# Kernel optimization log

Measured on AMD Instinct MI355X. Metric: run time of the kernel, lower is better.

The kernel has to match this reference:

```python
import jax, jax.numpy as jnp
import numpy as np


def setup_inputs() -> dict:
    key = jax.random.key(0)
    k1, k2 = jax.random.split(key)
    x = jax.random.normal(k1, (3000, 800, 8), dtype=jnp.float32)
    y = jax.random.normal(k2, (3000, 800, 8), dtype=jnp.float32)
    return {"x": x, "y": y}


def _cumtrapz(a):
    # torch.cumulative_trapezoid along last axis (unit spacing): len nt-1
    return jnp.cumsum(0.5 * (a[:, 1:] + a[:, :-1]), axis=1)


def _wd1d(x, y):
    nt = x.shape[0]
    # flatten (ntraces, nchannels) -> batch of independent 1D traces [N, nt]
    syn = x.reshape(nt, -1).T
    obs = y.reshape(nt, -1).T
    # per trace-pair joint minimum (torch.min(torch.min(syn), torch.min(obs)))
    mind = jnp.minimum(syn.min(axis=1, keepdims=True), obs.min(axis=1, keepdims=True))
    syn = syn - mind
    obs = obs - mind
    cdf_syn = _cumtrapz(syn)                                  # [N, nt-1]
    cdf_obs = _cumtrapz(obs)                                  # [N, nt-1]
    syn_norm = cdf_syn / jnp.sum(cdf_syn, axis=1, keepdims=True)
    obs_norm = cdf_obs / jnp.sum(cdf_obs, axis=1, keepdims=True)
    # torch.searchsorted default (right=False) == jnp side='left'
    idx = jax.vmap(lambda a, v: jnp.searchsorted(a, v, side='left'))(obs_norm, syn_norm)
    idx = jnp.minimum(idx, nt - 1)                            # clamp; t[idx] == idx since t = arange(nt)
    t_tail = jnp.arange(1, nt, dtype=jnp.int32)               # t[1:]
    diff = (t_tail[None, :] - idx).astype(syn_norm.dtype)
    return jnp.sum(diff * diff * syn_norm)


def reference(x, y):
    return _wd1d(x, y)
```

## Files before the change

kernel.cpp:

```cpp
#include <hip/hip_runtime.h>

#define NT   3000
#define NK   2999
#define NTR  6400
#define TRIW 4498500.0f
#define FINF 3.4e38f

#define TSTR 3008
#define CB   47

__device__ __forceinline__ float wave_incl_scan(float v, int lane) {
    #pragma unroll
    for (int d = 1; d < 64; d <<= 1) {
        float t = __shfl_up(v, d);
        if (lane >= d) v += t;
    }
    return v;
}
__device__ __forceinline__ float wave_red_add(float v) {
    #pragma unroll
    for (int d = 1; d < 64; d <<= 1) v += __shfl_xor(v, d);
    return v;
}
__device__ __forceinline__ float wave_red_min(float v) {
    #pragma unroll
    for (int d = 1; d < 64; d <<= 1) v = fminf(v, __shfl_xor(v, d));
    return v;
}

__global__ __launch_bounds__(256) void kT(
    const float* __restrict__ X, const float* __restrict__ Y,
    float* __restrict__ sTx, float* __restrict__ sTy,
    float* __restrict__ mnx, float* __restrict__ mny,
    float* __restrict__ wsx, float* __restrict__ wsy)
{
    __shared__ float t[65][65];
    const int lane = threadIdx.x & 63;
    const int wv   = threadIdx.x >> 6;
    const int n0 = blockIdx.x * 64;
    const int j0 = blockIdx.y * 64;
    const int z  = blockIdx.z;
    const float* __restrict__ src = z ? Y : X;
    float* __restrict__ dst = z ? sTy : sTx;
    float* __restrict__ mnA = z ? mny : mnx;
    float* __restrict__ wsA = z ? wsy : wsx;

    #pragma unroll
    for (int i = 0; i < 17; ++i) {
        const int r = wv + 4 * i;
        if (r < 65) {
            const int jr = j0 + r;
            if (jr < NT) t[r][lane] = src[(size_t)jr * NTR + n0 + lane];
        }
    }
    __syncthreads();

    const int j = j0 + lane;
    const bool vs = (j < NK);
    const bool va = (j < NT);
    const float w = vs ? (float)(NK - j) : 0.f;

    for (int rr = 0; rr < 16; ++rr) {
        const int row = wv * 16 + rr;
        const float a0 = t[lane][row];
        const float a1 = t[lane + 1][row];
        const float s  = vs ? 0.5f * (a0 + a1) : 0.f;
        dst[(size_t)(n0 + row) * TSTR + j0 + lane] = s;
        const float ws = wave_red_add(s * w);
        const float mv = wave_red_min(va ? a0 : FINF);
        if (lane == 0) {
            wsA[blockIdx.y * NTR + n0 + row] = ws;
            mnA[blockIdx.y * NTR + n0 + row] = mv;
        }
    }
}

__global__ __launch_bounds__(256) void kB2(
    const float* __restrict__ mnx, const float* __restrict__ mny,
    const float* __restrict__ wsx, const float* __restrict__ wsy,
    float* __restrict__ mindA, float* __restrict__ SsA, float* __restrict__ SoA)
{
    const int n = blockIdx.x * 256 + threadIdx.x;
    float mn = FINF, sx = 0.f, sy = 0.f;
    for (int c = 0; c < CB; ++c) {
        const int o = c * NTR + n;
        mn = fminf(mn, fminf(mnx[o], mny[o]));
        sx += wsx[o]; sy += wsy[o];
    }
    mindA[n] = mn;
    SsA[n] = sx - mn * TRIW;
    SoA[n] = sy - mn * TRIW;
}

__global__ __launch_bounds__(256) void kC2(
    const float* __restrict__ sTx, const float* __restrict__ sTy,
    const float* __restrict__ mindA, const float* __restrict__ SsA,
    const float* __restrict__ SoA, float* __restrict__ partial)
{
    const int lane = threadIdx.x & 63;
    const int wv   = threadIdx.x >> 6;
    const int n = blockIdx.x * 4 + wv;

    const float mind = mindA[n];
    const float Ss = SsA[n];
    const float So = SoA[n];
    const float* __restrict__ sx_row = sTx + (size_t)n * TSTR;
    const float* __restrict__ sy_row = sTy + (size_t)n * TSTR;

    int   m0 = 0;
    float co = 0.f;
    float ov;

    #define REFILL() do {                                                   \
        const int mm = m0 + lane;                                           \
        float v_ = (mm < NK) ? sy_row[mm] : 0.f;                            \
        float pf_ = wave_incl_scan(v_, lane);                               \
        ov = (mm < NK) ? (co + pf_ - (float)(mm + 1) * mind) * Ss : FINF;   \
        co += __shfl(pf_, 63);                                              \
    } while (0)

    REFILL();

    float cs = 0.f, acc = 0.f;
    for (int b = 0; b < CB; ++b) {
        const int j = b * 64 + lane;
        const bool valid = (j < NK);
        float v = valid ? sx_row[j] : 0.f;
        float pf = wave_incl_scan(v, lane);
        const float synp = cs + pf - (float)(j + 1) * mind;
        cs += __shfl(pf, 63);
        const float target = valid ? synp * So : -FINF;

        bool pend = true;
        int idx = 0;
        while (true) {
            const float ov_top = __shfl(ov, 63);
            int lo = 0;
            #pragma unroll
            for (int s = 32; s; s >>= 1) {
                const float pv = __shfl(ov, lo + s - 1);
                if (pv < target) lo += s;
            }
            if (pend && (target <= ov_top)) { idx = m0 + lo; pend = false; }
            if (__all(!pend)) break;
            m0 += 64;
            REFILL();
        }
        if (valid) {
            const float diff = (float)(j + 1 - idx);
            acc = fmaf(diff * diff, synp, acc);
        }
    }
    #undef REFILL

    const float tot = wave_red_add(acc);
    __shared__ float red[4];
    if (lane == 0) red[wv] = tot / Ss;
    __syncthreads();
    if (threadIdx.x == 0)
        partial[blockIdx.x] = red[0] + red[1] + red[2] + red[3];
}

__global__ __launch_bounds__(256) void kD(
    const float* __restrict__ partial, float* __restrict__ out)
{
    float v = 0.f;
    for (int i = threadIdx.x; i < 1600; i += 256) v += partial[i];
    __shared__ float red[256];
    red[threadIdx.x] = v;
    __syncthreads();
    for (int s = 128; s > 0; s >>= 1) {
        if (threadIdx.x < s) red[threadIdx.x] += red[threadIdx.x + s];
        __syncthreads();
    }
    if (threadIdx.x == 0) out[0] = red[0];
}

#define NPAIR  3200
#define FCH    64
#define FKCH   47
#define GRP    8
#define GT     64

__global__ __launch_bounds__(128) void fA(
    const float* __restrict__ X, const float* __restrict__ Y,
    float* __restrict__ offx, float* __restrict__ offy,
    float* __restrict__ cmn,
    float* __restrict__ wsxA, float* __restrict__ wsyA)
{
    const int p = blockIdx.x * 128 + threadIdx.x;
    const int n = 2 * p;
    const int c = blockIdx.y;
    const int j0 = c * FKCH;
    const int j1 = min(NK, j0 + FKCH);

    const float2* __restrict__ X2 = (const float2*)X;
    const float2* __restrict__ Y2 = (const float2*)Y;

    float2 xp = X2[j0 * NPAIR + p];
    float2 yp = Y2[j0 * NPAIR + p];
    float mn0 = fminf(xp.x, yp.x), mn1 = fminf(xp.y, yp.y);
    float sx0 = 0.f, sx1 = 0.f, sy0 = 0.f, sy1 = 0.f;
    float wx0 = 0.f, wx1 = 0.f, wy0 = 0.f, wy1 = 0.f;

    #pragma unroll 8
    for (int j = j0; j < j1; ++j) {
        const float2 xn = X2[(j + 1) * NPAIR + p];
        const float2 yn = Y2[(j + 1) * NPAIR + p];
        const float w = (float)(NK - j);
        float s;
        s = 0.5f * (xp.x + xn.x); sx0 += s; wx0 = fmaf(s, w, wx0);
        s = 0.5f * (xp.y + xn.y); sx1 += s; wx1 = fmaf(s, w, wx1);
        s = 0.5f * (yp.x + yn.x); sy0 += s; wy0 = fmaf(s, w, wy0);
        s = 0.5f * (yp.y + yn.y); sy1 += s; wy1 = fmaf(s, w, wy1);
        mn0 = fminf(mn0, fminf(xn.x, yn.x));
        mn1 = fminf(mn1, fminf(xn.y, yn.y));
        xp = xn; yp = yn;
    }

    const int o = c * NTR + n;
    *(float2*)&offx[o] = make_float2(sx0, sx1);
    *(float2*)&offy[o] = make_float2(sy0, sy1);
    *(float2*)&cmn[o]  = make_float2(mn0, mn1);
    atomicAdd(&wsxA[n], wx0); atomicAdd(&wsxA[n + 1], wx1);
    atomicAdd(&wsyA[n], wy0); atomicAdd(&wsyA[n + 1], wy1);
}

__global__ __launch_bounds__(256) void fB(
    float* __restrict__ offx, float* __restrict__ offy,
    const float* __restrict__ cmn,
    const float* __restrict__ wsxA, const float* __restrict__ wsyA,
    float* __restrict__ mindA, float* __restrict__ SsynA,
    float* __restrict__ SobsA, float* __restrict__ out)
{
    __shared__ float tA[FCH][GT + 1];
    __shared__ float tB[FCH][GT + 1];

    const int n0 = blockIdx.x * GT;
    const int tid = threadIdx.x;
    const int lane = tid & 63;
    const int crow = tid >> 6;
    if (blockIdx.x == 0 && tid == 0) out[0] = 0.0f;

    for (int c = crow; c < FCH; c += 4)
        tB[c][lane] = cmn[c * NTR + n0 + lane];
    __syncthreads();
    if (tid < GT) {
        float mn = FINF;
        for (int c = 0; c < FCH; ++c) mn = fminf(mn, tB[c][tid]);
        mindA[n0 + tid] = mn;
        SsynA[n0 + tid] = wsxA[n0 + tid] - mn * TRIW;
        SobsA[n0 + tid] = wsyA[n0 + tid] - mn * TRIW;
    }
    __syncthreads();

    for (int c = crow; c < FCH; c += 4) {
        tA[c][lane] = offx[c * NTR + n0 + lane];
        tB[c][lane] = offy[c * NTR + n0 + lane];
    }
    __syncthreads();
    if (tid < GT) {
        float rx = 0.f, ry = 0.f;
        for (int c = 0; c < FCH; ++c) {
            const float tx = tA[c][tid], ty = tB[c][tid];
            tA[c][tid] = rx; tB[c][tid] = ry;
            rx += tx; ry += ty;
        }
    }
    __syncthreads();
    for (int c = crow; c < FCH; c += 4) {
        offx[c * NTR + n0 + lane] = tA[c][lane];
        offy[c * NTR + n0 + lane] = tB[c][lane];
    }
}

__global__ __launch_bounds__(256) void fC(
    const float* __restrict__ X, const float* __restrict__ Y,
    const float* __restrict__ offx, const float* __restrict__ offy,
    const float* __restrict__ mindA, const float* __restrict__ SsynA,
    const float* __restrict__ SobsA, float* __restrict__ out)
{
    const int n = blockIdx.x * 256 + threadIdx.x;
    const int c = blockIdx.y;
    const int j0 = c * FKCH;
    const int j1 = min(NK, j0 + FKCH);

    const float mind = mindA[n];
    const float Ssyn = SsynA[n];
    const float Sobs = SobsA[n];
    const float invS = 1.0f / Ssyn;

    float cs = offx[c * NTR + n];
    float xp = X[j0 * NTR + n];
    float acc = 0.f;

    int   mbase;
    float co, ylast;
    float o[GRP];
    float co8, y8;

    #define FILL() do {                                                   \
        float yl_ = ylast, cc_ = co;                                      \
        _Pragma("unroll")                                                 \
        for (int i = 0; i < GRP; ++i) {                                   \
            const int m_ = mbase + i;                                     \
            const int ml_ = (m_ < NK) ? (m_ + 1) : NK;                    \
            const float yn_ = Y[ml_ * NTR + n];                           \
            cc_ += 0.5f * (yl_ + yn_);                                    \
            yl_ = yn_;                                                    \
            const float v_ = (cc_ - (float)(m_ + 1) * mind) * Ssyn;       \
            o[i] = (m_ < NK) ? v_ : FINF;                                 \
        }                                                                 \
        co8 = cc_; y8 = yl_;                                              \
    } while (0)

    #define COUNT(tgt, cnt) do {                                          \
        cnt = 0;                                                          \
        _Pragma("unroll")                                                 \
        for (int i = 0; i < GRP; ++i) cnt += (o[i] < (tgt)) ? 1 : 0;      \
    } while (0)

    {
        const float xn = X[(j0 + 1) * NTR + n];
        cs += 0.5f * (xp + xn); xp = xn;
        const float synp = cs - (float)(j0 + 1) * mind;
        const float target = synp * Sobs;

        int cc = 0;
        for (int c2 = min(FCH - 1, c + 2); c2 >= 1; --c2) {
            const float v = (offy[c2 * NTR + n] - (float)(c2 * FKCH) * mind) * Ssyn;
            if (v < target) { cc = c2; break; }
        }
        mbase = cc * FKCH;
        co = offy[cc * NTR + n];
        ylast = Y[mbase * NTR + n];
        FILL();
        int cnt; COUNT(target, cnt);
        while (cnt == GRP) {
            mbase += GRP; co = co8; ylast = y8;
            FILL();
            COUNT(target, cnt);
        }
        const float diff = (float)(j0 + 1 - (mbase + cnt));
        acc = fmaf(diff * diff, synp, acc);
    }

    for (int k = j0 + 1; k < j1; ++k) {
        const float xn = X[(k + 1) * NTR + n];
        cs += 0.5f * (xp + xn); xp = xn;
        const float synp = cs - (float)(k + 1) * mind;
        const float target = synp * Sobs;

        int cnt; COUNT(target, cnt);
        while (cnt == GRP) {
            mbase += GRP; co = co8; ylast = y8;
            FILL();
            COUNT(target, cnt);
        }
        const float diff = (float)(k + 1 - (mbase + cnt));
        acc = fmaf(diff * diff, synp, acc);
    }
    acc *= invS;

    #undef FILL
    #undef COUNT

    __shared__ float red[256];
    red[threadIdx.x] = acc;
    __syncthreads();
    for (int s = 128; s > 0; s >>= 1) {
        if (threadIdx.x < s) red[threadIdx.x] += red[threadIdx.x + s];
        __syncthreads();
    }
    if (threadIdx.x == 0) atomicAdd(out, red[0]);
}

extern "C" void kernel_launch(void* const* d_in, const int* in_sizes, int n_in,
                              void* d_out, int out_size, void* d_ws, size_t ws_size,
                              hipStream_t stream)
{
    const float* X = (const float*)d_in[0];
    const float* Y = (const float*)d_in[1];
    float* out = (float*)d_out;

    const size_t NEW_REQ =
        ((size_t)2 * NTR * TSTR + 4 * (size_t)CB * NTR + 3 * NTR + 1600) * 4;

    if (ws_size >= NEW_REQ) {
        float* w = (float*)d_ws;
        float* sTx = w;
        float* sTy = sTx + (size_t)NTR * TSTR;
        float* mnx = sTy + (size_t)NTR * TSTR;
        float* mny = mnx + CB * NTR;
        float* wsx = mny + CB * NTR;
        float* wsy = wsx + CB * NTR;
        float* mindA = wsy + CB * NTR;
        float* SsA = mindA + NTR;
        float* SoA = SsA + NTR;
        float* partial = SoA + NTR;

        kT<<<dim3(100, 47, 2), 256, 0, stream>>>(X, Y, sTx, sTy, mnx, mny, wsx, wsy);
        kB2<<<25, 256, 0, stream>>>(mnx, mny, wsx, wsy, mindA, SsA, SoA);
        kC2<<<1600, 256, 0, stream>>>(sTx, sTy, mindA, SsA, SoA, partial);
        kD<<<1, 256, 0, stream>>>(partial, out);
    } else {
        float* w = (float*)d_ws;
        float* offx  = w;
        float* offy  = offx + FCH * NTR;
        float* cmn   = offy + FCH * NTR;
        float* wsxA  = cmn  + FCH * NTR;
        float* wsyA  = wsxA + NTR;
        float* mindA = wsyA + NTR;
        float* SsynA = mindA + NTR;
        float* SobsA = SsynA + NTR;

        hipMemsetAsync(wsxA, 0, 2 * NTR * sizeof(float), stream);

        dim3 gA(NPAIR / 128, FCH), bA(128);
        dim3 gB(NTR / GT), bB(256);
        dim3 gC(NTR / 256, FCH), bC(256);
        fA<<<gA, bA, 0, stream>>>(X, Y, offx, offy, cmn, wsxA, wsyA);
        fB<<<gB, bB, 0, stream>>>(offx, offy, cmn, wsxA, wsyA,
                                  mindA, SsynA, SobsA, out);
        fC<<<gC, bC, 0, stream>>>(X, Y, offx, offy, mindA, SsynA, SobsA, out);
    }
}
```

Measured before the change: 358.6 us.

## Split per-trace Wasserstein scan into segments with precomputed chunk prefixes and search starts

kT now writes per-chunk plain sums of the trapezoid values, folds the weighted sums into per-trace atomics, and reduces the per-trace minimum with an order-preserving unsigned atomicMin. kB2 turns the chunk sums into exclusive prefixes and coarsely locates a starting obs chunk for each of 8 segments. kC2 then runs 8 independent waves per trace, each starting from its precomputed prefix and search position, instead of one wave doing the whole serial scan. The aim is to cut the long serial per-trace loop and raise parallelism. The cost is extra memsets, atomics and a small extra pass, and float prefix sums are now added in a different order.

```diff
diff --git a/kernel.cpp b/kernel.cpp
--- a/kernel.cpp
+++ b/kernel.cpp
@@ -8,6 +8,10 @@
 
 #define TSTR 3008
 #define CB   47
+#define NSEG 8
+#define SEGB 6
+#define GT   64
+#define NCBLK 3200
 
 __device__ __forceinline__ float wave_incl_scan(float v, int lane) {
     #pragma unroll
@@ -22,19 +26,24 @@
     for (int d = 1; d < 64; d <<= 1) v += __shfl_xor(v, d);
     return v;
 }
-__device__ __forceinline__ float wave_red_min(float v) {
-    #pragma unroll
-    for (int d = 1; d < 64; d <<= 1) v = fminf(v, __shfl_xor(v, d));
-    return v;
+__device__ __forceinline__ unsigned fmap(float f) {
+    unsigned u = __float_as_uint(f);
+    return (u & 0x80000000u) ? ~u : (u | 0x80000000u);
+}
+__device__ __forceinline__ float funmap(unsigned u) {
+    u = (u & 0x80000000u) ? (u & 0x7FFFFFFFu) : ~u;
+    return __uint_as_float(u);
 }
 
 __global__ __launch_bounds__(256) void kT(
     const float* __restrict__ X, const float* __restrict__ Y,
     float* __restrict__ sTx, float* __restrict__ sTy,
-    float* __restrict__ mnx, float* __restrict__ mny,
-    float* __restrict__ wsx, float* __restrict__ wsy)
+    float* __restrict__ ssx, float* __restrict__ ssy,
+    float* __restrict__ wsxA, float* __restrict__ wsyA,
+    unsigned* __restrict__ mnUx, unsigned* __restrict__ mnUy)
 {
     __shared__ float t[65][65];
+    __shared__ float pS[4][GT], pW[4][GT], pM[4][GT];
     const int lane = threadIdx.x & 63;
     const int wv   = threadIdx.x >> 6;
     const int n0 = blockIdx.x * 64;
@@ -42,8 +51,9 @@
     const int z  = blockIdx.z;
     const float* __restrict__ src = z ? Y : X;
     float* __restrict__ dst = z ? sTy : sTx;
-    float* __restrict__ mnA = z ? mny : mnx;
-    float* __restrict__ wsA = z ? wsy : wsx;
+    float* __restrict__ ssA = z ? ssy : ssx;
+    float* __restrict__ wA  = z ? wsyA : wsxA;
+    unsigned* __restrict__ mU = z ? mnUy : mnUx;
 
     #pragma unroll
     for (int i = 0; i < 17; ++i) {
@@ -57,49 +67,105 @@
 
     const int j = j0 + lane;
     const bool vs = (j < NK);
-    const bool va = (j < NT);
-    const float w = vs ? (float)(NK - j) : 0.f;
-
     for (int rr = 0; rr < 16; ++rr) {
         const int row = wv * 16 + rr;
         const float a0 = t[lane][row];
         const float a1 = t[lane + 1][row];
-        const float s  = vs ? 0.5f * (a0 + a1) : 0.f;
-        dst[(size_t)(n0 + row) * TSTR + j0 + lane] = s;
-        const float ws = wave_red_add(s * w);
-        const float mv = wave_red_min(va ? a0 : FINF);
-        if (lane == 0) {
-            wsA[blockIdx.y * NTR + n0 + row] = ws;
-            mnA[blockIdx.y * NTR + n0 + row] = mv;
-        }
+        dst[(size_t)(n0 + row) * TSTR + j0 + lane] = vs ? 0.5f * (a0 + a1) : 0.f;
+    }
+
+    {
+        const int r0 = wv * 16;
+        float sum = 0.f, wsum = 0.f, mn = FINF;
+        float aprev = t[r0][lane];
+        #pragma unroll 4
+        for (int rr = 0; rr < 16; ++rr) {
+            const int jr = j0 + r0 + rr;
+            const float anext = t[r0 + rr + 1][lane];
+            if (jr < NT) mn = fminf(mn, aprev);
+            if (jr < NK) {
+                const float s = 0.5f * (aprev + anext);
+                sum += s;
+                wsum = fmaf(s, (float)(NK - jr), wsum);
+            }
+            aprev = anext;
+        }
+        pS[wv][lane] = sum; pW[wv][lane] = wsum; pM[wv][lane] = mn;
+    }
+    __syncthreads();
+    if (threadIdx.x < GT) {
+        const int l = threadIdx.x;
+        const float S = pS[0][l] + pS[1][l] + pS[2][l] + pS[3][l];
+        const float W = pW[0][l] + pW[1][l] + pW[2][l] + pW[3][l];
+        const float M = fminf(fminf(pM[0][l], pM[1][l]), fminf(pM[2][l], pM[3][l]));
+        ssA[blockIdx.y * NTR + n0 + l] = S;
+        atomicAdd(&wA[n0 + l], W);
+        atomicMin(&mU[n0 + l], fmap(M));
     }
 }
 
 __global__ __launch_bounds__(256) void kB2(
-    const float* __restrict__ mnx, const float* __restrict__ mny,
-    const float* __restrict__ wsx, const float* __restrict__ wsy,
-    float* __restrict__ mindA, float* __restrict__ SsA, float* __restrict__ SoA)
-{
-    const int n = blockIdx.x * 256 + threadIdx.x;
-    float mn = FINF, sx = 0.f, sy = 0.f;
-    for (int c = 0; c < CB; ++c) {
-        const int o = c * NTR + n;
-        mn = fminf(mn, fminf(mnx[o], mny[o]));
-        sx += wsx[o]; sy += wsy[o];
-    }
-    mindA[n] = mn;
-    SsA[n] = sx - mn * TRIW;
-    SoA[n] = sy - mn * TRIW;
-}
-
-__global__ __launch_bounds__(256) void kC2(
+    float* __restrict__ ssx, float* __restrict__ ssy,
+    const float* __restrict__ wsxA, const float* __restrict__ wsyA,
+    const unsigned* __restrict__ mnUx, const unsigned* __restrict__ mnUy,
+    float* __restrict__ mindA, float* __restrict__ SsA, float* __restrict__ SoA,
+    unsigned char* __restrict__ qstA)
+{
+    __shared__ float tA[CB][GT + 1];
+    __shared__ float tB[CB][GT + 1];
+    const int n0 = blockIdx.x * GT;
+    const int tid = threadIdx.x, lane = tid & 63, crow = tid >> 6;
+
+    for (int c = crow; c < CB; c += 4) {
+        tA[c][lane] = ssx[c * NTR + n0 + lane];
+        tB[c][lane] = ssy[c * NTR + n0 + lane];
+    }
+    __syncthreads();
+
+    if (tid < GT) {
+        const float mn = fminf(funmap(mnUx[n0 + tid]), funmap(mnUy[n0 + tid]));
+        const float Ss = wsxA[n0 + tid] - mn * TRIW;
+        const float So = wsyA[n0 + tid] - mn * TRIW;
+        mindA[n0 + tid] = mn; SsA[n0 + tid] = Ss; SoA[n0 + tid] = So;
+
+        float rx = 0.f, ry = 0.f;
+        for (int c = 0; c < CB; ++c) {
+            const float tx = tA[c][tid], ty = tB[c][tid];
+            tA[c][tid] = rx; tB[c][tid] = ry;
+            rx += tx; ry += ty;
+        }
+        int q = 0;
+        for (int s = 0; s < NSEG; ++s) {
+            const int c0 = s * SEGB;
+            const float tgt = (tA[c0][tid] - (float)(c0 * 64) * mn) * So;
+            while (q + 1 < CB) {
+                const float ov = (tB[q + 1][tid] - (float)((q + 1) * 64) * mn) * Ss;
+                if (ov < tgt) ++q; else break;
+            }
+            qstA[s * NTR + n0 + tid] = (unsigned char)q;
+        }
+    }
+    __syncthreads();
+    for (int c = crow; c < CB; c += 4) {
+        ssx[c * NTR + n0 + lane] = tA[c][lane];
+        ssy[c * NTR + n0 + lane] = tB[c][lane];
+    }
+}
+
+__global__ __launch_bounds__(1024) void kC2(
     const float* __restrict__ sTx, const float* __restrict__ sTy,
+    const float* __restrict__ ssxS, const float* __restrict__ ssyS,
     const float* __restrict__ mindA, const float* __restrict__ SsA,
-    const float* __restrict__ SoA, float* __restrict__ partial)
+    const float* __restrict__ SoA, const unsigned char* __restrict__ qstA,
+    float* __restrict__ partial)
 {
     const int lane = threadIdx.x & 63;
     const int wv   = threadIdx.x >> 6;
-    const int n = blockIdx.x * 4 + wv;
+    const int task = blockIdx.x * 16 + wv;
+    const int n    = task >> 3;
+    const int seg  = task & (NSEG - 1);
+    const int c0   = seg * SEGB;
+    const int cend = min(CB, c0 + SEGB);
 
     const float mind = mindA[n];
     const float Ss = SsA[n];
@@ -107,9 +173,14 @@
     const float* __restrict__ sx_row = sTx + (size_t)n * TSTR;
     const float* __restrict__ sy_row = sTy + (size_t)n * TSTR;
 
-    int   m0 = 0;
-    float co = 0.f;
-    float ov;
+    float cs = ssxS[c0 * NTR + n];
+    int   m0;
+    float co, ov;
+    {
+        const int q = (int)qstA[seg * NTR + n];
+        m0 = q * 64;
+        co = ssyS[q * NTR + n];
+    }
 
     #define REFILL() do {                                                   \
         const int mm = m0 + lane;                                           \
@@ -121,8 +192,8 @@
 
     REFILL();
 
-    float cs = 0.f, acc = 0.f;
-    for (int b = 0; b < CB; ++b) {
+    float acc = 0.f;
+    for (int b = c0; b < cend; ++b) {
         const int j = b * 64 + lane;
         const bool valid = (j < NK);
         float v = valid ? sx_row[j] : 0.f;
@@ -153,19 +224,23 @@
     }
     #undef REFILL
 
-    const float tot = wave_red_add(acc);
-    __shared__ float red[4];
-    if (lane == 0) red[wv] = tot / Ss;
-    __syncthreads();
-    if (threadIdx.x == 0)
-        partial[blockIdx.x] = red[0] + red[1] + red[2] + red[3];
+    const float tot = wave_red_add(acc) / Ss;
+    __shared__ float red[16];
+    if (lane == 0) red[wv] = tot;
+    __syncthreads();
+    if (threadIdx.x < 64) {
+        float v = (threadIdx.x < 16) ? red[threadIdx.x] : 0.f;
+        #pragma unroll
+        for (int d = 1; d < 16; d <<= 1) v += __shfl_xor(v, d);
+        if (threadIdx.x == 0) partial[blockIdx.x] = v;
+    }
 }
 
 __global__ __launch_bounds__(256) void kD(
     const float* __restrict__ partial, float* __restrict__ out)
 {
     float v = 0.f;
-    for (int i = threadIdx.x; i < 1600; i += 256) v += partial[i];
+    for (int i = threadIdx.x; i < NCBLK; i += 256) v += partial[i];
     __shared__ float red[256];
     red[threadIdx.x] = v;
     __syncthreads();
@@ -180,7 +255,6 @@
 #define FCH    64
 #define FKCH   47
 #define GRP    8
-#define GT     64
 
 __global__ __launch_bounds__(128) void fA(
     const float* __restrict__ X, const float* __restrict__ Y,
@@ -384,24 +458,33 @@
     float* out = (float*)d_out;
 
     const size_t NEW_REQ =
-        ((size_t)2 * NTR * TSTR + 4 * (size_t)CB * NTR + 3 * NTR + 1600) * 4;
+        ((size_t)2 * NTR * TSTR + 2 * (size_t)CB * NTR + 7 * NTR + NCBLK
+         + (NSEG * NTR) / 4 + 16) * 4;
 
     if (ws_size >= NEW_REQ) {
         float* w = (float*)d_ws;
-        float* sTx = w;
-        float* sTy = sTx + (size_t)NTR * TSTR;
-        float* mnx = sTy + (size_t)NTR * TSTR;
-        float* mny = mnx + CB * NTR;
-        float* wsx = mny + CB * NTR;
-        float* wsy = wsx + CB * NTR;
-        float* mindA = wsy + CB * NTR;
-        float* SsA = mindA + NTR;
-        float* SoA = SsA + NTR;
+        float* sTx  = w;
+        float* sTy  = sTx + (size_t)NTR * TSTR;
+        float* ssx  = sTy + (size_t)NTR * TSTR;
+        float* ssy  = ssx + CB * NTR;
+        float* wsxA = ssy + CB * NTR;
+        float* wsyA = wsxA + NTR;
+        unsigned* mnU = (unsigned*)(wsyA + NTR);
+        float* mindA = (float*)(mnU + 2 * NTR);
+        float* SsA   = mindA + NTR;
+        float* SoA   = SsA + NTR;
         float* partial = SoA + NTR;
-
-        kT<<<dim3(100, 47, 2), 256, 0, stream>>>(X, Y, sTx, sTy, mnx, mny, wsx, wsy);
-        kB2<<<25, 256, 0, stream>>>(mnx, mny, wsx, wsy, mindA, SsA, SoA);
-        kC2<<<1600, 256, 0, stream>>>(sTx, sTy, mindA, SsA, SoA, partial);
+        unsigned char* qstA = (unsigned char*)(partial + NCBLK);
+
+        hipMemsetAsync(wsxA, 0, 2 * NTR * sizeof(float), stream);
+        hipMemsetAsync(mnU, 0xFF, 2 * NTR * sizeof(unsigned), stream);
+
+        kT<<<dim3(100, 47, 2), 256, 0, stream>>>(X, Y, sTx, sTy, ssx, ssy,
+                                                 wsxA, wsyA, mnU, mnU + NTR);
+        kB2<<<100, 256, 0, stream>>>(ssx, ssy, wsxA, wsyA, mnU, mnU + NTR,
+                                     mindA, SsA, SoA, qstA);
+        kC2<<<NCBLK, 1024, 0, stream>>>(sTx, sTy, ssx, ssy,
+                                        mindA, SsA, SoA, qstA, partial);
         kD<<<1, 256, 0, stream>>>(partial, out);
     } else {
         float* w = (float*)d_ws;
```

After: 331.7 us. 1.08x faster.
